# Kernel tuning notes

Measured on AMD Instinct MI355X. Metric: run time of the kernel, lower is better.

## Reference

```python
import jax, jax.numpy as jnp
import numpy as np

K = 40          # neighbors, from __init__ default
EPS_BN = 1e-5   # BatchNorm eps; eval mode with running_mean=0, running_var=1


def knn_idx(x, k):
    # x: (B, C, N) -> indices (B, N, k) of k nearest neighbors (incl. self)
    xx = jnp.sum(x * x, axis=1)                      # (B, N)
    inner = jnp.einsum('bcn,bcm->bnm', x, x)         # (B, N, N)
    neg_dist = 2.0 * inner - xx[:, :, None] - xx[:, None, :]
    return jax.lax.top_k(neg_dist, k)[1]


def get_graph_feature(x, k):
    # DGCNN dynamic graph feature: (B, C, N) -> (B, 2C, N, k)
    idx = knn_idx(x, k)                              # (B, N, k) int
    xt = jnp.transpose(x, (0, 2, 1))                 # (B, N, C)
    nbr = jax.vmap(lambda f, i: f[i])(xt, idx)       # (B, N, k, C)
    ctr = xt[:, :, None, :]
    feat = jnp.concatenate([nbr - ctr, jnp.broadcast_to(ctr, nbr.shape)], axis=-1)
    return jnp.transpose(feat, (0, 3, 1, 2))         # (B, 2C, N, k)


def bn_affine(x, g, b, ch_axis=1):
    # eval-mode BatchNorm with running_mean=0, running_var=1
    shape = [1] * x.ndim
    shape[ch_axis] = -1
    scale = (g / jnp.sqrt(1.0 + EPS_BN)).reshape(shape)
    return x * scale + b.reshape(shape)


def conv_bn_lrelu2d(x, w, g, b):
    # 1x1 Conv2d (no bias) + BN2d + LeakyReLU(0.2); x: (B, Cin, N, k)
    y = jnp.einsum('oi,bink->bonk', w, x)
    return jax.nn.leaky_relu(bn_affine(y, g, b, 1), 0.2)


def sa_layer(x, qk, vw, vb, tw, tb, g, b):
    # PCT-style offset self-attention; q and k share weights. x: (B, C, N)
    xq = jnp.einsum('oc,bcn->bno', qk, x)            # (B, N, C/4)
    xk = jnp.einsum('oc,bcn->bon', qk, x)            # (B, C/4, N)
    xv = jnp.einsum('oc,bcn->bon', vw, x) + vb[None, :, None]
    energy = jnp.einsum('bno,bom->bnm', xq, xk)      # (B, N, N)
    attn = jax.nn.softmax(energy, axis=-1)
    attn = attn / (1e-9 + jnp.sum(attn, axis=1, keepdims=True))
    xr = jnp.einsum('bcn,bnm->bcm', xv, attn)        # (B, C, N)
    d = x - xr
    dr = jnp.einsum('oc,bcn->bon', tw, d) + tb[None, :, None]
    return x + jax.nn.relu(bn_affine(dr, g, b, 1))


def setup_inputs() -> dict:
    key = jax.random.key(0)
    ks = jax.random.split(key, 16)
    s = 0.05
    d = {
        'x': jax.random.normal(ks[0], (8, 2048, 3), jnp.float32),
        'w1': jax.random.normal(ks[1], (64, 6), jnp.float32) * s,
        'g1': jnp.ones((64,), jnp.float32), 'b1': jnp.zeros((64,), jnp.float32),
        'w2': jax.random.normal(ks[2], (64, 64), jnp.float32) * s,
        'g2': jnp.ones((64,), jnp.float32), 'b2': jnp.zeros((64,), jnp.float32),
        'w3': jax.random.normal(ks[3], (64, 128), jnp.float32) * s,
        'g3': jnp.ones((64,), jnp.float32), 'b3': jnp.zeros((64,), jnp.float32),
        'w4': jax.random.normal(ks[4], (64, 64), jnp.float32) * s,
        'g4': jnp.ones((64,), jnp.float32), 'b4': jnp.zeros((64,), jnp.float32),
        'w5': jax.random.normal(ks[5], (64, 128), jnp.float32) * s,
        'g5': jnp.ones((64,), jnp.float32), 'b5': jnp.zeros((64,), jnp.float32),
        'sa_qk': jax.random.normal(ks[6], (4, 32, 128), jnp.float32) * s,
        'sa_v': jax.random.normal(ks[7], (4, 128, 128), jnp.float32) * s,
        'sa_vb': jnp.zeros((4, 128), jnp.float32),
        'sa_t': jax.random.normal(ks[8], (4, 128, 128), jnp.float32) * s,
        'sa_tb': jnp.zeros((4, 128), jnp.float32),
        'sa_g': jnp.ones((4, 128), jnp.float32),
        'sa_b': jnp.zeros((4, 128), jnp.float32),
        'fuse_w': jax.random.normal(ks[9], (256, 512), jnp.float32) * s,
        'fuse_g': jnp.ones((256,), jnp.float32),
        'fuse_b': jnp.zeros((256,), jnp.float32),
    }
    return d


def reference(x, w1, g1, b1, w2, g2, b2, w3, g3, b3, w4, g4, b4, w5, g5, b5,
              sa_qk, sa_v, sa_vb, sa_t, sa_tb, sa_g, sa_b,
              fuse_w, fuse_g, fuse_b):
    xc = jnp.transpose(x, (0, 2, 1))                 # (B, 3, N)
    f = get_graph_feature(xc, K)                     # (B, 6, N, k)
    f = conv_bn_lrelu2d(f, w1, g1, b1)
    f = conv_bn_lrelu2d(f, w2, g2, b2)
    x1 = jnp.max(f, axis=-1)                         # (B, 64, N)
    f = get_graph_feature(x1, K)                     # (B, 128, N, k)
    f = conv_bn_lrelu2d(f, w3, g3, b3)
    f = conv_bn_lrelu2d(f, w4, g4, b4)
    x2 = jnp.max(f, axis=-1)                         # (B, 64, N)
    h = jnp.concatenate([x1, x2], axis=1)            # (B, 128, N)
    outs = []
    for i in range(4):
        h = sa_layer(h, sa_qk[i], sa_v[i], sa_vb[i], sa_t[i], sa_tb[i], sa_g[i], sa_b[i])
        outs.append(h)
    cat = jnp.concatenate(outs, axis=1)              # (B, 512, N)
    y = jnp.einsum('oi,bin->bon', fuse_w, cat)       # (B, 256, N)
    return jax.nn.leaky_relu(bn_affine(y, fuse_g, fuse_b, 1), 0.2)
```

## Files before the change

kernel.cpp:

```cpp
#include <hip/hip_runtime.h>

#define Bb 8
#define Nn 2048
#define Kk 40
#define HS (128*Nn)

__device__ __forceinline__ unsigned f2o(float f){
  unsigned u = __float_as_uint(f);
  return (u & 0x80000000u) ? ~u : (u | 0x80000000u);
}

__device__ __forceinline__ void wave_top40(float* d, int lane, int* op){
  float gv[4]; int gs[4];
  #pragma unroll
  for (int g=0; g<4; ++g){
    float bv = d[g*8]; int bs = g*8;
    #pragma unroll
    for (int j=1;j<8;++j){
      float v = d[g*8+j];
      if (v > bv){ bv = v; bs = g*8+j; }
    }
    gv[g]=bv; gs[g]=bs;
  }
  for (int t=0; t<Kk; ++t){
    float bv = gv[0]; int bs = gs[0];
    if (gv[1] > bv){ bv=gv[1]; bs=gs[1]; }
    if (gv[2] > bv){ bv=gv[2]; bs=gs[2]; }
    if (gv[3] > bv){ bv=gv[3]; bs=gs[3]; }
    int bm = bs*64 + lane;
    unsigned long long key = ((unsigned long long)f2o(bv) << 32) | (unsigned)(~bm);
    #pragma unroll
    for (int s=32;s>0;s>>=1){
      unsigned long long o = __shfl_xor(key, s, 64);
      if (o > key) key = o;
    }
    int wm = (int)(~(unsigned)key);
    if (lane == 0) op[t] = wm;
    bool mine = ((wm & 63) == lane);
    int wsl = wm >> 6;
    if (mine){
      int G = wsl >> 3;
      #pragma unroll
      for (int g=0; g<4; ++g){
        if (g == G){
          float nv = -__builtin_inff(); int ns = g*8;
          #pragma unroll
          for (int j=0;j<8;++j){
            float v = d[g*8+j];
            if (g*8+j == wsl) v = -__builtin_inff();
            d[g*8+j] = v;
            if (v > nv){ nv=v; ns=g*8+j; }
          }
          gv[g]=nv; gs[g]=ns;
        }
      }
    }
  }
}

__device__ __forceinline__ void wave_top40_g(float* d, int lane, int* op){
  float gv[4]; int gs[4];
  #pragma unroll
  for (int g=0; g<4; ++g){
    float bv = d[g*8]; int bs = g*8;
    #pragma unroll
    for (int j=1;j<8;++j){
      float v = d[g*8+j];
      if (v > bv){ bv = v; bs = g*8+j; }
    }
    gv[g]=bv; gs[g]=bs;
  }
  for (int t=0; t<Kk; ++t){
    float bv = gv[0]; int bs = gs[0];
    if (gv[1] > bv){ bv=gv[1]; bs=gs[1]; }
    if (gv[2] > bv){ bv=gv[2]; bs=gs[2]; }
    if (gv[3] > bv){ bv=gv[3]; bs=gs[3]; }
    int bm = ((bs>>2)<<8) + lane*4 + (bs&3);
    unsigned long long key = ((unsigned long long)f2o(bv) << 32) | (unsigned)(~bm);
    #pragma unroll
    for (int s=32;s>0;s>>=1){
      unsigned long long o = __shfl_xor(key, s, 64);
      if (o > key) key = o;
    }
    int wm = (int)(~(unsigned)key);
    if (lane == 0) op[t] = wm;
    bool mine = (((wm>>2) & 63) == lane);
    int wsl = ((wm>>8)<<2) | (wm & 3);
    if (mine){
      int G = wsl >> 3;
      #pragma unroll
      for (int g=0; g<4; ++g){
        if (g == G){
          float nv = -__builtin_inff(); int ns = g*8;
          #pragma unroll
          for (int j=0;j<8;++j){
            float v = d[g*8+j];
            if (g*8+j == wsl) v = -__builtin_inff();
            d[g*8+j] = v;
            if (v > nv){ nv=v; ns=g*8+j; }
          }
          gv[g]=nv; gs[g]=ns;
        }
      }
    }
  }
}

__global__ __launch_bounds__(256) void k_xx1(const float* __restrict__ x, float* __restrict__ XX){
  int e = blockIdx.x*256 + threadIdx.x;
  if (e >= Bb*Nn) return;
  float p0 = x[e*3+0], p1 = x[e*3+1], p2 = x[e*3+2];
  XX[e] = __fadd_rn(__fadd_rn(__fmul_rn(p0,p0), __fmul_rn(p1,p1)), __fmul_rn(p2,p2));
}

__global__ __launch_bounds__(256) void k_prep_wt(const float* __restrict__ w1, const float* __restrict__ w2,
                                                 const float* __restrict__ w3, const float* __restrict__ w4,
                                                 const float* __restrict__ fw,
                                                 float* __restrict__ W1T, float* __restrict__ W2T,
                                                 float* __restrict__ W3T, float* __restrict__ W4T,
                                                 float* __restrict__ FWT){
  int e = blockIdx.x*256 + threadIdx.x;
  if (e < 384)   { int i=e/64,  c=e%64;  W1T[e] = w1[c*6+i];    return; } e -= 384;
  if (e < 4096)  { int i=e/64,  c=e%64;  W2T[e] = w2[c*64+i];   return; } e -= 4096;
  if (e < 8192)  { int i=e/64,  c=e%64;  W3T[e] = w3[c*128+i];  return; } e -= 8192;
  if (e < 4096)  { int i=e/64,  c=e%64;  W4T[e] = w4[c*64+i];   return; } e -= 4096;
  if (e < 131072){ int i=e/256, o=e%256; FWT[e] = fw[o*512+i];  return; }
}

__global__ __launch_bounds__(256) void k_knn1(const float* __restrict__ P, const float* __restrict__ XX,
                                              int* __restrict__ IDX){
  int blk = blockIdx.x;
  int b = blk >> 9;
  int w = threadIdx.x >> 6, lane = threadIdx.x & 63;
  int n = (blk & 511)*4 + w;
  const float* Pb = P + b*Nn*3;
  const float* xb = XX + b*Nn;
  __shared__ float Pl[Nn*3];
  __shared__ float Xl[Nn];
  for (int e = threadIdx.x; e < Nn*3; e += 256) Pl[e] = Pb[e];
  for (int e = threadIdx.x; e < Nn; e += 256) Xl[e] = xb[e];
  __syncthreads();
  float c0 = Pl[n*3+0], c1 = Pl[n*3+1], c2 = Pl[n*3+2];
  float xn = Xl[n];
  float d[32];
  #pragma unroll
  for (int j=0;j<32;++j){
    int m = j*64 + lane;
    float a0 = Pl[m*3+0], a1 = Pl[m*3+1], a2 = Pl[m*3+2];
    float in_ = __fadd_rn(__fadd_rn(__fmul_rn(c0,a0), __fmul_rn(c1,a1)), __fmul_rn(c2,a2));
    d[j] = __fsub_rn(__fsub_rn(__fmul_rn(2.0f,in_), xn), Xl[m]);
  }
  wave_top40(d, lane, IDX + (b*Nn+n)*Kk);
}

__global__ __launch_bounds__(64) void k_ec1(const float* __restrict__ P, const int* __restrict__ IDX,
                                            const float* __restrict__ W1T, const float* __restrict__ W2T,
                                            const float* __restrict__ g1, const float* __restrict__ b1,
                                            const float* __restrict__ g2, const float* __restrict__ b2,
                                            float* __restrict__ X1T){
  int e = blockIdx.x;
  int b = e >> 11;
  int lane = threadIdx.x;
  __shared__ float dC[Kk*4];
  __shared__ __align__(16) float y1L[64*44];
  float c0 = P[e*3+0], c1 = P[e*3+1], c2 = P[e*3+2];
  if (lane < Kk) {
    int idx = IDX[e*Kk + lane] & (Nn-1);
    const float* pn = P + (b*Nn + idx)*3;
    dC[lane*4+0] = __fsub_rn(pn[0], c0);
    dC[lane*4+1] = __fsub_rn(pn[1], c1);
    dC[lane*4+2] = __fsub_rn(pn[2], c2);
  }
  __syncthreads();
  float w10 = W1T[0*64+lane], w11 = W1T[1*64+lane], w12 = W1T[2*64+lane];
  float w13 = W1T[3*64+lane], w14 = W1T[4*64+lane], w15 = W1T[5*64+lane];
  float p3 = __fmul_rn(w13,c0), p4 = __fmul_rn(w14,c1), p5 = __fmul_rn(w15,c2);
  float s1 = __fdiv_rn(g1[lane], __fsqrt_rn(1.0f + 1e-5f));
  float o1 = b1[lane];
  for (int k=0;k<Kk;++k){
    float t = __fmul_rn(w10, dC[k*4+0]);
    t = __fadd_rn(t, __fmul_rn(w11, dC[k*4+1]));
    t = __fadd_rn(t, __fmul_rn(w12, dC[k*4+2]));
    t = __fadd_rn(t, p3); t = __fadd_rn(t, p4); t = __fadd_rn(t, p5);
    float y = __fadd_rn(__fmul_rn(t, s1), o1);
    y = (y >= 0.0f) ? y : __fmul_rn(0.2f, y);
    y1L[lane*44+k] = y;
  }
  __syncthreads();
  float4 q[10];
  #pragma unroll
  for (int k4=0;k4<10;++k4) q[k4] = make_float4(0.f,0.f,0.f,0.f);
  for (int i=0;i<64;++i){
    float w = W2T[i*64+lane];
    const float4* yp = (const float4*)&y1L[i*44];
    #pragma unroll
    for (int k4=0;k4<10;++k4){
      float4 yv = yp[k4];
      q[k4].x = __fadd_rn(q[k4].x, __fmul_rn(w, yv.x));
      q[k4].y = __fadd_rn(q[k4].y, __fmul_rn(w, yv.y));
      q[k4].z = __fadd_rn(q[k4].z, __fmul_rn(w, yv.z));
      q[k4].w = __fadd_rn(q[k4].w, __fmul_rn(w, yv.w));
    }
  }
  float s2 = __fdiv_rn(g2[lane], __fsqrt_rn(1.0f + 1e-5f));
  float o2 = b2[lane];
  float mx = -__builtin_inff();
  #pragma unroll
  for (int k4=0;k4<10;++k4){
    float vs[4] = {q[k4].x, q[k4].y, q[k4].z, q[k4].w};
    #pragma unroll
    for (int j=0;j<4;++j){
      float y = __fadd_rn(__fmul_rn(vs[j], s2), o2);
      y = (y >= 0.0f) ? y : __fmul_rn(0.2f, y);
      mx = fmaxf(mx, y);
    }
  }
  X1T[e*64 + lane] = mx;
}

__global__ __launch_bounds__(256) void k_xx2(const float* __restrict__ X1T, float* __restrict__ XX2){
  int e = blockIdx.x*256 + threadIdx.x;
  const float* r = X1T + e*64;
  float a = 0.f;
  for (int c=0;c<64;++c) a = __fadd_rn(a, __fmul_rn(r[c], r[c]));
  XX2[e] = a;
}

__global__ __launch_bounds__(256) void k_knn2(const float* __restrict__ X1C, const float* __restrict__ XX2,
                                              int* __restrict__ IDX){
  int blk = blockIdx.x;
  int b = blk >> 8;
  int n0 = (blk & 255) << 3;
  int w = threadIdx.x >> 6, lane = threadIdx.x & 63;
  __shared__ float qL[8*64];
  for (int e=threadIdx.x; e<512; e+=256){
    int q = e >> 6, c = e & 63;
    qL[e] = X1C[b*HS + c*Nn + n0 + q];
  }
  __syncthreads();
  float4 a0[8], a1[8];
  #pragma unroll
  for (int j=0;j<8;++j){
    a0[j] = make_float4(0.f,0.f,0.f,0.f);
    a1[j] = make_float4(0.f,0.f,0.f,0.f);
  }
  for (int c=0;c<64;++c){
    const float4* row = (const float4*)(X1C + b*HS + c*Nn);
    float q0 = qL[(w*2+0)*64 + c];
    float q1 = qL[(w*2+1)*64 + c];
    #pragma unroll
    for (int j=0;j<8;++j){
      float4 v = row[j*64 + lane];
      a0[j].x = __fadd_rn(a0[j].x, __fmul_rn(q0, v.x));
      a0[j].y = __fadd_rn(a0[j].y, __fmul_rn(q0, v.y));
      a0[j].z = __fadd_rn(a0[j].z, __fmul_rn(q0, v.z));
      a0[j].w = __fadd_rn(a0[j].w, __fmul_rn(q0, v.w));
      a1[j].x = __fadd_rn(a1[j].x, __fmul_rn(q1, v.x));
      a1[j].y = __fadd_rn(a1[j].y, __fmul_rn(q1, v.y));
      a1[j].z = __fadd_rn(a1[j].z, __fmul_rn(q1, v.z));
      a1[j].w = __fadd_rn(a1[j].w, __fmul_rn(q1, v.w));
    }
  }
  const float* xb = XX2 + b*Nn;
  const float4* xb4 = (const float4*)xb;
  {
    int n = n0 + w*2 + 0;
    float xn = xb[n];
    float d[32];
    #pragma unroll
    for (int j=0;j<8;++j){
      float4 xm = xb4[j*64 + lane];
      d[j*4+0] = __fsub_rn(__fsub_rn(__fmul_rn(2.0f, a0[j].x), xn), xm.x);
      d[j*4+1] = __fsub_rn(__fsub_rn(__fmul_rn(2.0f, a0[j].y), xn), xm.y);
      d[j*4+2] = __fsub_rn(__fsub_rn(__fmul_rn(2.0f, a0[j].z), xn), xm.z);
      d[j*4+3] = __fsub_rn(__fsub_rn(__fmul_rn(2.0f, a0[j].w), xn), xm.w);
    }
    wave_top40_g(d, lane, IDX + (b*Nn + n)*Kk);
  }
  {
    int n = n0 + w*2 + 1;
    float xn = xb[n];
    float d[32];
    #pragma unroll
    for (int j=0;j<8;++j){
      float4 xm = xb4[j*64 + lane];
      d[j*4+0] = __fsub_rn(__fsub_rn(__fmul_rn(2.0f, a1[j].x), xn), xm.x);
      d[j*4+1] = __fsub_rn(__fsub_rn(__fmul_rn(2.0f, a1[j].y), xn), xm.y);
      d[j*4+2] = __fsub_rn(__fsub_rn(__fmul_rn(2.0f, a1[j].z), xn), xm.z);
      d[j*4+3] = __fsub_rn(__fsub_rn(__fmul_rn(2.0f, a1[j].w), xn), xm.w);
    }
    wave_top40_g(d, lane, IDX + (b*Nn + n)*Kk);
  }
}

__global__ __launch_bounds__(64) void k_ec2(const float* __restrict__ X1T, const int* __restrict__ IDX,
                                            const float* __restrict__ W3T, const float* __restrict__ W4T,
                                            const float* __restrict__ g3, const float* __restrict__ b3,
                                            const float* __restrict__ g4, const float* __restrict__ b4,
                                            float* __restrict__ X2T){
  int e = blockIdx.x; int b = e >> 11; int lane = threadIdx.x;
  __shared__ __align__(16) float dL[64*44];
  __shared__ float ctrL[64];
  float ctr = X1T[e*64 + lane];
  ctrL[lane] = ctr;
  __syncthreads();
  for (int k=0;k<Kk;++k){
    int idx = IDX[e*Kk + k] & (Nn-1);
    dL[lane*44 + k] = X1T[(b*Nn+idx)*64 + lane] - ctr;
  }
  __syncthreads();
  float base = 0.f;
  for (int i=0;i<64;++i) base = fmaf(W3T[(64+i)*64 + lane], ctrL[i], base);
  float4 q[10];
  #pragma unroll
  for (int k4=0;k4<10;++k4) q[k4] = make_float4(base,base,base,base);
  for (int i=0;i<64;++i){
    float w = W3T[i*64 + lane];
    const float4* dp = (const float4*)&dL[i*44];
    #pragma unroll
    for (int k4=0;k4<10;++k4){
      float4 d = dp[k4];
      q[k4].x = fmaf(w, d.x, q[k4].x);
      q[k4].y = fmaf(w, d.y, q[k4].y);
      q[k4].z = fmaf(w, d.z, q[k4].z);
      q[k4].w = fmaf(w, d.w, q[k4].w);
    }
  }
  float s3 = g3[lane] / sqrtf(1.0f+1e-5f);
  float o3 = b3[lane];
  __syncthreads();
  #pragma unroll
  for (int k4=0;k4<10;++k4){
    float4 y;
    y.x = q[k4].x*s3 + o3; y.x = (y.x>=0.f)?y.x:0.2f*y.x;
    y.y = q[k4].y*s3 + o3; y.y = (y.y>=0.f)?y.y:0.2f*y.y;
    y.z = q[k4].z*s3 + o3; y.z = (y.z>=0.f)?y.z:0.2f*y.z;
    y.w = q[k4].w*s3 + o3; y.w = (y.w>=0.f)?y.w:0.2f*y.w;
    *(float4*)&dL[lane*44 + k4*4] = y;
  }
  __syncthreads();
  float4 p[10];
  #pragma unroll
  for (int k4=0;k4<10;++k4) p[k4] = make_float4(0.f,0.f,0.f,0.f);
  for (int i=0;i<64;++i){
    float w = W4T[i*64 + lane];
    const float4* yp = (const float4*)&dL[i*44];
    #pragma unroll
    for (int k4=0;k4<10;++k4){
      float4 yv = yp[k4];
      p[k4].x = fmaf(w, yv.x, p[k4].x);
      p[k4].y = fmaf(w, yv.y, p[k4].y);
      p[k4].z = fmaf(w, yv.z, p[k4].z);
      p[k4].w = fmaf(w, yv.w, p[k4].w);
    }
  }
  float s4 = g4[lane] / sqrtf(1.0f+1e-5f);
  float o4 = b4[lane];
  float mx = -__builtin_inff();
  #pragma unroll
  for (int k4=0;k4<10;++k4){
    float vs[4] = {p[k4].x, p[k4].y, p[k4].z, p[k4].w};
    #pragma unroll
    for (int j=0;j<4;++j){
      float y = vs[j]*s4 + o4;
      y = (y>=0.f)?y:0.2f*y;
      mx = fmaxf(mx, y);
    }
  }
  X2T[e*64 + lane] = mx;
}

__global__ __launch_bounds__(256) void k_tr(const float* __restrict__ src, float* __restrict__ dst){
  int b = blockIdx.x >> 5; int n0 = (blockIdx.x & 31) << 6;
  __shared__ float t[64*65];
  for (int e=threadIdx.x; e<4096; e+=256){
    int r = e >> 6, c = e & 63;
    t[r*65+c] = src[(b*Nn + n0 + r)*64 + c];
  }
  __syncthreads();
  for (int e=threadIdx.x; e<4096; e+=256){
    int c = e >> 6, r = e & 63;
    dst[b*HS + c*Nn + n0 + r] = t[r*65+c];
  }
}

__global__ __launch_bounds__(256) void k_sa_a(const float* __restrict__ IN,
                                              const float* __restrict__ QKw, const float* __restrict__ Vw,
                                              const float* __restrict__ Vb,
                                              float* __restrict__ QX, float* __restrict__ XV){
  int blk = blockIdx.x;
  int part = blk & 1; int nt = (blk >> 1) & 31; int b = blk >> 6;
  int n0 = nt << 6;
  int w = threadIdx.x >> 6, lane = threadIdx.x & 63;
  __shared__ __align__(16) float xl[128*64];
  for (int e=threadIdx.x; e<2048; e+=256){
    int c = e >> 4, j4 = (e & 15) << 2;
    *(float4*)&xl[(c<<6) + j4] = *(const float4*)&IN[b*HS + c*Nn + n0 + j4];
  }
  __syncthreads();
  for (int i=0;i<20;++i){
    int r = part*80 + w*20 + i;
    const float4* wp4;
    if (r < 32) wp4 = (const float4*)(QKw + r*128);
    else        wp4 = (const float4*)(Vw + (r-32)*128);
    float a = 0.f;
    #pragma unroll
    for (int c4=0;c4<32;++c4){
      float4 wv = wp4[c4];
      a = fmaf(wv.x, xl[(c4*4+0)*64 + lane], a);
      a = fmaf(wv.y, xl[(c4*4+1)*64 + lane], a);
      a = fmaf(wv.z, xl[(c4*4+2)*64 + lane], a);
      a = fmaf(wv.w, xl[(c4*4+3)*64 + lane], a);
    }
    if (r < 32) QX[(b*32+r)*Nn + n0 + lane] = a;
    else { int o = r-32; XV[(b*128+o)*Nn + n0 + lane] = a + Vb[o]; }
  }
}

__global__ __launch_bounds__(256) void k_sa_b(const float* __restrict__ QX,
                                              float* __restrict__ RMP, float* __restrict__ RSP){
  int blk = blockIdx.x;
  int b = blk >> 6, sub = blk & 63;
  int ncn = sub >> 3, mcn = sub & 7;
  int n = ncn*256 + threadIdx.x;
  float q[32];
  #pragma unroll
  for (int o=0;o<32;++o) q[o] = QX[(b*32+o)*Nn + n];
  __shared__ __align__(16) float qt[32*128];
  float mr = -__builtin_inff(), lr = 0.f;
  int m0 = mcn*256;
  for (int t=0;t<2;++t){
    for (int e=threadIdx.x; e<1024; e+=256){
      int o = e >> 5, mm4 = (e & 31) << 2;
      *(float4*)&qt[(o<<7) + mm4] = *(const float4*)&QX[(b*32+o)*Nn + m0 + t*128 + mm4];
    }
    __syncthreads();
    for (int mm=0;mm<128;mm+=4){
      float e0=0.f, e1=0.f, e2=0.f, e3=0.f;
      #pragma unroll
      for (int o=0;o<32;++o){
        float qo=q[o];
        float4 qv = *(const float4*)&qt[o*128+mm];
        e0 = fmaf(qo, qv.x, e0);
        e1 = fmaf(qo, qv.y, e1);
        e2 = fmaf(qo, qv.z, e2);
        e3 = fmaf(qo, qv.w, e3);
      }
      if (e0 > mr){ lr = lr*expf(mr-e0) + 1.f; mr = e0; } else lr += expf(e0-mr);
      if (e1 > mr){ lr = lr*expf(mr-e1) + 1.f; mr = e1; } else lr += expf(e1-mr);
      if (e2 > mr){ lr = lr*expf(mr-e2) + 1.f; mr = e2; } else lr += expf(e2-mr);
      if (e3 > mr){ lr = lr*expf(mr-e3) + 1.f; mr = e3; } else lr += expf(e3-mr);
    }
    __syncthreads();
  }
  RMP[(b*Nn+n)*8 + mcn] = mr;
  RSP[(b*Nn+n)*8 + mcn] = lr;
}

__global__ __launch_bounds__(256) void k_sa_b2(const float* __restrict__ RMP, const float* __restrict__ RSP,
                                               float* __restrict__ RMX, float* __restrict__ RSM){
  int e = blockIdx.x*256 + threadIdx.x;
  float M = -__builtin_inff();
  #pragma unroll
  for (int i=0;i<8;++i) M = fmaxf(M, RMP[e*8+i]);
  float l = 0.f;
  #pragma unroll
  for (int i=0;i<8;++i) l += RSP[e*8+i]*expf(RMP[e*8+i]-M);
  RMX[e] = M; RSM[e] = l;
}

#define SM_QM 0
#define SM_QN 1024
#define SM_XV 2048
#define SM_SL 6272
#define SM_MX 7296
#define SM_RL 7328

__global__ __launch_bounds__(256) void k_sa_cm(const float* __restrict__ QX, const float* __restrict__ XV,
                                               const float* __restrict__ RMAX, const float* __restrict__ RSUM,
                                               float* __restrict__ PP, float* __restrict__ CSP){
  int blk = blockIdx.x;
  int part = blk & 1, mt = (blk >> 1) & 63, b = blk >> 7;
  int m0 = mt << 5;
  int tid = threadIdx.x;
  int nnp = tid >> 4, mmp = tid & 15;
  int tc = tid >> 3, tm8 = tid & 7;
  __shared__ __align__(16) float sm[7360];
  {
    int o = tid >> 3, mm4 = (tid & 7) << 2;
    *(float4*)&sm[SM_QM + (o<<5) + mm4] = *(const float4*)&QX[(b*32+o)*Nn + m0 + mm4];
  }
  float acc[4][4];
  #pragma unroll
  for (int ci=0;ci<4;++ci){
    #pragma unroll
    for (int mi=0;mi<4;++mi) acc[ci][mi] = 0.f;
  }
  float csr = 0.f;
  int it0 = part*32;
  for (int it=it0; it<it0+32; ++it){
    int nb = it*32;
    __syncthreads();
    {
      int o = tid >> 3, nn4 = (tid & 7) << 2;
      *(float4*)&sm[SM_QN + (o<<5) + nn4] = *(const float4*)&QX[(b*32+o)*Nn + nb + nn4];
    }
    for (int e=tid; e<1024; e+=256){
      int c = e >> 3, nn4 = (e & 7) << 2;
      float4 v = *(const float4*)&XV[(b*128+c)*Nn + nb + nn4];
      sm[SM_XV + (nn4+0)*132 + c] = v.x;
      sm[SM_XV + (nn4+1)*132 + c] = v.y;
      sm[SM_XV + (nn4+2)*132 + c] = v.z;
      sm[SM_XV + (nn4+3)*132 + c] = v.w;
    }
    if (tid < 32){ sm[SM_MX+tid] = RMAX[b*Nn + nb + tid]; sm[SM_RL+tid] = 1.0f / RSUM[b*Nn + nb + tid]; }
    __syncthreads();
    float e00=0.f, e01=0.f, e10=0.f, e11=0.f;
    #pragma unroll
    for (int o=0;o<32;++o){
      float2 qn = *(const float2*)&sm[SM_QN + o*32 + nnp*2];
      float2 qm = *(const float2*)&sm[SM_QM + o*32 + mmp*2];
      e00 = fmaf(qn.x, qm.x, e00);
      e01 = fmaf(qn.x, qm.y, e01);
      e10 = fmaf(qn.y, qm.x, e10);
      e11 = fmaf(qn.y, qm.y, e11);
    }
    float mx0 = sm[SM_MX + nnp*2],   rl0 = sm[SM_RL + nnp*2];
    float mx1 = sm[SM_MX + nnp*2+1], rl1 = sm[SM_RL + nnp*2+1];
    float2 s0; s0.x = expf(e00-mx0)*rl0; s0.y = expf(e01-mx0)*rl0;
    float2 s1; s1.x = expf(e10-mx1)*rl1; s1.y = expf(e11-mx1)*rl1;
    *(float2*)&sm[SM_SL + (nnp*2  )*32 + mmp*2] = s0;
    *(float2*)&sm[SM_SL + (nnp*2+1)*32 + mmp*2] = s1;
    __syncthreads();
    if (tid < 32){
      #pragma unroll
      for (int nn=0;nn<32;++nn) csr += sm[SM_SL + nn*32 + tid];
    }
    #pragma unroll 8
    for (int nn=0;nn<32;++nn){
      float4 xv4 = *(const float4*)&sm[SM_XV + nn*132 + tc*4];
      float4 s4  = *(const float4*)&sm[SM_SL + nn*32  + tm8*4];
      acc[0][0] = fmaf(xv4.x, s4.x, acc[0][0]);
      acc[0][1] = fmaf(xv4.x, s4.y, acc[0][1]);
      acc[0][2] = fmaf(xv4.x, s4.z, acc[0][2]);
      acc[0][3] = fmaf(xv4.x, s4.w, acc[0][3]);
      acc[1][0] = fmaf(xv4.y, s4.x, acc[1][0]);
      acc[1][1] = fmaf(xv4.y, s4.y, acc[1][1]);
      acc[1][2] = fmaf(xv4.y, s4.z, acc[1][2]);
      acc[1][3] = fmaf(xv4.y, s4.w, acc[1][3]);
      acc[2][0] = fmaf(xv4.z, s4.x, acc[2][0]);
      acc[2][1] = fmaf(xv4.z, s4.y, acc[2][1]);
      acc[2][2] = fmaf(xv4.z, s4.z, acc[2][2]);
      acc[2][3] = fmaf(xv4.z, s4.w, acc[2][3]);
      acc[3][0] = fmaf(xv4.w, s4.x, acc[3][0]);
      acc[3][1] = fmaf(xv4.w, s4.y, acc[3][1]);
      acc[3][2] = fmaf(xv4.w, s4.z, acc[3][2]);
      acc[3][3] = fmaf(xv4.w, s4.w, acc[3][3]);
    }
  }
  int slot = (b*64 + mt)*2 + part;
  #pragma unroll
  for (int ci=0;ci<4;++ci){
    int c = tc*4 + ci;
    *(float4*)&PP[slot*4096 + c*32 + tm8*4] =
      make_float4(acc[ci][0], acc[ci][1], acc[ci][2], acc[ci][3]);
  }
  if (tid < 32) CSP[slot*32 + tid] = csr;
}

__global__ __launch_bounds__(256) void k_sa_cc(const float* IN,
                                               const float* __restrict__ PP, const float* __restrict__ CSP,
                                               const float* __restrict__ Tw, const float* __restrict__ Tb,
                                               const float* __restrict__ Gs, const float* __restrict__ Bs,
                                               float* OUT){
  int blk = blockIdx.x;
  int mt = blk & 63, b = blk >> 6;
  int m0 = mt << 5;
  int tid = threadIdx.x;
  int tc = tid >> 3, tm8 = tid & 7;
  __shared__ __align__(16) float sm[4128];
  int s0 = (b*64 + mt)*2, s1 = s0 + 1;
  if (tid < 32) sm[4096 + tid] = CSP[s0*32 + tid] + CSP[s1*32 + tid];
  __syncthreads();
  #pragma unroll
  for (int ci=0;ci<4;++ci){
    int c = tc*4 + ci;
    float4 p0 = *(const float4*)&PP[s0*4096 + c*32 + tm8*4];
    float4 p1 = *(const float4*)&PP[s1*4096 + c*32 + tm8*4];
    float4 inv = *(const float4*)&IN[b*HS + c*Nn + m0 + tm8*4];
    float am[4] = {p0.x+p1.x, p0.y+p1.y, p0.z+p1.z, p0.w+p1.w};
    float ivs[4] = {inv.x, inv.y, inv.z, inv.w};
    #pragma unroll
    for (int mi=0;mi<4;++mi){
      int ml = tm8*4 + mi;
      float cs = sm[4096 + ml];
      float xr = am[mi] / (1e-9f + cs);
      sm[c*32 + ml] = ivs[mi] - xr;
    }
  }
  __syncthreads();
  int hw = tid >> 5, m = tid & 31;
  float sroot = sqrtf(1.0f + 1e-5f);
  for (int oo=0; oo<16; ++oo){
    int o = oo*8 + hw;
    const float4* twp = (const float4*)(Tw + o*128);
    float a = 0.f;
    #pragma unroll
    for (int c4=0;c4<32;++c4){
      float4 wv = twp[c4];
      a = fmaf(wv.x, sm[(c4*4+0)*32 + m], a);
      a = fmaf(wv.y, sm[(c4*4+1)*32 + m], a);
      a = fmaf(wv.z, sm[(c4*4+2)*32 + m], a);
      a = fmaf(wv.w, sm[(c4*4+3)*32 + m], a);
    }
    a += Tb[o];
    float y = a * (Gs[o] / sroot) + Bs[o];
    y = fmaxf(y, 0.f);
    OUT[b*HS + o*Nn + m0 + m] = IN[b*HS + o*Nn + m0 + m] + y;
  }
}

__global__ __launch_bounds__(256) void k_fuse_part(const float* __restrict__ Hc, const float* __restrict__ FWT,
                                                   float* __restrict__ ACC, int l, int init, int fin,
                                                   const float* __restrict__ FGF, const float* __restrict__ FBF){
  int blk = blockIdx.x;
  int hf = blk & 1; int nt = (blk >> 1) & 31; int b = blk >> 6;
  int n0 = nt << 6;
  int w = threadIdx.x >> 6, lane = threadIdx.x & 63;
  __shared__ __align__(16) float xt[128*64];
  for (int e=threadIdx.x; e<2048; e+=256){
    int c = e >> 4, j4 = (e & 15) << 2;
    *(float4*)&xt[(c<<6) + j4] = *(const float4*)&Hc[(b*128 + c)*Nn + n0 + j4];
  }
  __syncthreads();
  float4 a[8];
  #pragma unroll
  for (int j=0;j<8;++j) a[j] = make_float4(0.f,0.f,0.f,0.f);
  int ob = hf*128 + w*32;
  for (int c=0;c<128;++c){
    float xv = xt[c*64 + lane];
    const float4* wr = (const float4*)(FWT + (l*128+c)*256 + ob);
    #pragma unroll
    for (int j4=0;j4<8;++j4){
      float4 wv = wr[j4];
      a[j4].x = fmaf(wv.x, xv, a[j4].x);
      a[j4].y = fmaf(wv.y, xv, a[j4].y);
      a[j4].z = fmaf(wv.z, xv, a[j4].z);
      a[j4].w = fmaf(wv.w, xv, a[j4].w);
    }
  }
  float sroot = sqrtf(1.0f + 1e-5f);
  #pragma unroll
  for (int j4=0;j4<8;++j4){
    float vs[4] = {a[j4].x, a[j4].y, a[j4].z, a[j4].w};
    #pragma unroll
    for (int qq=0;qq<4;++qq){
      int o = ob + j4*4 + qq;
      int idx = (b*256 + o)*Nn + n0 + lane;
      float v = init ? vs[qq] : (ACC[idx] + vs[qq]);
      if (fin){
        float y = v * (FGF[o] / sroot) + FBF[o];
        y = (y >= 0.f) ? y : 0.2f*y;
        ACC[idx] = y;
      } else {
        ACC[idx] = v;
      }
    }
  }
}

extern "C" void kernel_launch(void* const* d_in, const int* in_sizes, int n_in,
                              void* d_out, int out_size, void* d_ws, size_t ws_size,
                              hipStream_t stream) {
  const float* X   = (const float*)d_in[0];
  const float* w1  = (const float*)d_in[1];
  const float* g1  = (const float*)d_in[2];
  const float* b1  = (const float*)d_in[3];
  const float* w2  = (const float*)d_in[4];
  const float* g2  = (const float*)d_in[5];
  const float* b2_ = (const float*)d_in[6];
  const float* w3  = (const float*)d_in[7];
  const float* g3  = (const float*)d_in[8];
  const float* b3  = (const float*)d_in[9];
  const float* w4  = (const float*)d_in[10];
  const float* g4  = (const float*)d_in[11];
  const float* b4  = (const float*)d_in[12];
  const float* qk  = (const float*)d_in[16];
  const float* sv  = (const float*)d_in[17];
  const float* svb = (const float*)d_in[18];
  const float* st  = (const float*)d_in[19];
  const float* stb = (const float*)d_in[20];
  const float* sg  = (const float*)d_in[21];
  const float* sb  = (const float*)d_in[22];
  const float* fw  = (const float*)d_in[23];
  const float* fg  = (const float*)d_in[24];
  const float* fb  = (const float*)d_in[25];

  float* ws = (float*)d_ws;
  float* H    = ws + 0;
  float* QXb  = ws + 2097152;
  float* XVb  = ws + 2621440;
  float* RMP  = ws + 4718592;
  float* RSP  = ws + 4849664;
  float* RMX  = ws + 4980736;
  float* RSM  = ws + 4997120;
  float* XX   = ws + 2146304;
  int*   IDX  = (int*)(ws + 2162688);
  float* X1T  = ws + 2818048;
  float* X2T  = ws + 3866624;
  float* C0   = ws + 5013504;
  float* W1T = C0 + 0;
  float* W2T = C0 + 384;
  float* W3T = C0 + 4480;
  float* W4T = C0 + 12672;
  float* FWT = C0 + 16768;
  float* PP  = ws + 5161344;
  float* CSP = ws + 9355648;
  float* ACC = (float*)d_out;

  k_xx1<<<64,256,0,stream>>>(X, XX);
  k_prep_wt<<<578,256,0,stream>>>(w1,w2,w3,w4,fw, W1T,W2T,W3T,W4T,FWT);
  k_knn1<<<4096,256,0,stream>>>(X, XX, IDX);
  k_ec1<<<16384,64,0,stream>>>(X, IDX, W1T, W2T, g1,b1,g2,b2_, X1T);
  k_xx2<<<64,256,0,stream>>>(X1T, XX);
  k_tr<<<256,256,0,stream>>>(X1T, H);
  k_knn2<<<2048,256,0,stream>>>(H, XX, IDX);
  k_ec2<<<16384,64,0,stream>>>(X1T, IDX, W3T, W4T, g3,b3,g4,b4, X2T);
  k_tr<<<256,256,0,stream>>>(X2T, H + 64*Nn);

  for (int l=0;l<4;++l){
    k_sa_a<<<512,256,0,stream>>>(H, qk + l*4096, sv + l*16384, svb + l*128, QXb, XVb);
    k_sa_b<<<512,256,0,stream>>>(QXb, RMP, RSP);
    k_sa_b2<<<64,256,0,stream>>>(RMP, RSP, RMX, RSM);
    k_sa_cm<<<1024,256,0,stream>>>(QXb, XVb, RMX, RSM, PP, CSP);
    k_sa_cc<<<512,256,0,stream>>>(H, PP, CSP,
                                  st + l*16384, stb + l*128, sg + l*128, sb + l*128, H);
    k_fuse_part<<<512,256,0,stream>>>(H, FWT, ACC, l, (l==0)?1:0, (l==3)?1:0, fg, fb);
  }
}
```

Baseline: 2.461 ms.

## Interleave two top-k selections and register-prefetch attention tiles

The kNN kernel now runs the two rows' top-40 selections interleaved in one routine, so the shuffle reductions of two independent chains overlap and hide latency. The attention kernel prefetches the next tile's Q, V and row-stat values into registers during the current tile's compute, then stores them to shared memory at the next iteration. Both changes raise register pressure, which may reduce occupancy.

Result: no change. 2.429 ms (-1.3%).

```diff
diff --git a/kernel.cpp b/kernel.cpp
--- a/kernel.cpp
+++ b/kernel.cpp
@@ -58,48 +58,85 @@
   }
 }
 
-__device__ __forceinline__ void wave_top40_g(float* d, int lane, int* op){
-  float gv[4]; int gs[4];
+__device__ __forceinline__ void wave_top40_g2(float* d0, float* d1, int lane,
+                                              int* op0, int* op1){
+  float gv0[4], gv1[4]; int gs0[4], gs1[4];
   #pragma unroll
   for (int g=0; g<4; ++g){
-    float bv = d[g*8]; int bs = g*8;
+    float bv0 = d0[g*8]; int bs0 = g*8;
+    float bv1 = d1[g*8]; int bs1 = g*8;
     #pragma unroll
     for (int j=1;j<8;++j){
-      float v = d[g*8+j];
-      if (v > bv){ bv = v; bs = g*8+j; }
-    }
-    gv[g]=bv; gs[g]=bs;
+      float v0 = d0[g*8+j];
+      if (v0 > bv0){ bv0 = v0; bs0 = g*8+j; }
+      float v1 = d1[g*8+j];
+      if (v1 > bv1){ bv1 = v1; bs1 = g*8+j; }
+    }
+    gv0[g]=bv0; gs0[g]=bs0;
+    gv1[g]=bv1; gs1[g]=bs1;
   }
   for (int t=0; t<Kk; ++t){
-    float bv = gv[0]; int bs = gs[0];
-    if (gv[1] > bv){ bv=gv[1]; bs=gs[1]; }
-    if (gv[2] > bv){ bv=gv[2]; bs=gs[2]; }
-    if (gv[3] > bv){ bv=gv[3]; bs=gs[3]; }
-    int bm = ((bs>>2)<<8) + lane*4 + (bs&3);
-    unsigned long long key = ((unsigned long long)f2o(bv) << 32) | (unsigned)(~bm);
+    float bv0 = gv0[0]; int bs0 = gs0[0];
+    if (gv0[1] > bv0){ bv0=gv0[1]; bs0=gs0[1]; }
+    if (gv0[2] > bv0){ bv0=gv0[2]; bs0=gs0[2]; }
+    if (gv0[3] > bv0){ bv0=gv0[3]; bs0=gs0[3]; }
+    float bv1 = gv1[0]; int bs1 = gs1[0];
+    if (gv1[1] > bv1){ bv1=gv1[1]; bs1=gs1[1]; }
+    if (gv1[2] > bv1){ bv1=gv1[2]; bs1=gs1[2]; }
+    if (gv1[3] > bv1){ bv1=gv1[3]; bs1=gs1[3]; }
+    int bm0 = ((bs0>>2)<<8) + lane*4 + (bs0&3);
+    int bm1 = ((bs1>>2)<<8) + lane*4 + (bs1&3);
+    unsigned long long key0 = ((unsigned long long)f2o(bv0) << 32) | (unsigned)(~bm0);
+    unsigned long long key1 = ((unsigned long long)f2o(bv1) << 32) | (unsigned)(~bm1);
     #pragma unroll
     for (int s=32;s>0;s>>=1){
-      unsigned long long o = __shfl_xor(key, s, 64);
-      if (o > key) key = o;
-    }
-    int wm = (int)(~(unsigned)key);
-    if (lane == 0) op[t] = wm;
-    bool mine = (((wm>>2) & 63) == lane);
-    int wsl = ((wm>>8)<<2) | (wm & 3);
-    if (mine){
-      int G = wsl >> 3;
-      #pragma unroll
-      for (int g=0; g<4; ++g){
-        if (g == G){
-          float nv = -__builtin_inff(); int ns = g*8;
-          #pragma unroll
-          for (int j=0;j<8;++j){
-            float v = d[g*8+j];
-            if (g*8+j == wsl) v = -__builtin_inff();
-            d[g*8+j] = v;
-            if (v > nv){ nv=v; ns=g*8+j; }
+      unsigned long long o0 = __shfl_xor(key0, s, 64);
+      unsigned long long o1 = __shfl_xor(key1, s, 64);
+      if (o0 > key0) key0 = o0;
+      if (o1 > key1) key1 = o1;
+    }
+    int wm0 = (int)(~(unsigned)key0);
+    int wm1 = (int)(~(unsigned)key1);
+    if (lane == 0){ op0[t] = wm0; op1[t] = wm1; }
+    {
+      bool mine = (((wm0>>2) & 63) == lane);
+      int wsl = ((wm0>>8)<<2) | (wm0 & 3);
+      if (mine){
+        int G = wsl >> 3;
+        #pragma unroll
+        for (int g=0; g<4; ++g){
+          if (g == G){
+            float nv = -__builtin_inff(); int ns = g*8;
+            #pragma unroll
+            for (int j=0;j<8;++j){
+              float v = d0[g*8+j];
+              if (g*8+j == wsl) v = -__builtin_inff();
+              d0[g*8+j] = v;
+              if (v > nv){ nv=v; ns=g*8+j; }
+            }
+            gv0[g]=nv; gs0[g]=ns;
           }
-          gv[g]=nv; gs[g]=ns;
+        }
+      }
+    }
+    {
+      bool mine = (((wm1>>2) & 63) == lane);
+      int wsl = ((wm1>>8)<<2) | (wm1 & 3);
+      if (mine){
+        int G = wsl >> 3;
+        #pragma unroll
+        for (int g=0; g<4; ++g){
+          if (g == G){
+            float nv = -__builtin_inff(); int ns = g*8;
+            #pragma unroll
+            for (int j=0;j<8;++j){
+              float v = d1[g*8+j];
+              if (g*8+j == wsl) v = -__builtin_inff();
+              d1[g*8+j] = v;
+              if (v > nv){ nv=v; ns=g*8+j; }
+            }
+            gv1[g]=nv; gs1[g]=ns;
+          }
         }
       }
     }
@@ -263,34 +300,24 @@
   }
   const float* xb = XX2 + b*Nn;
   const float4* xb4 = (const float4*)xb;
-  {
-    int n = n0 + w*2 + 0;
-    float xn = xb[n];
-    float d[32];
-    #pragma unroll
-    for (int j=0;j<8;++j){
-      float4 xm = xb4[j*64 + lane];
-      d[j*4+0] = __fsub_rn(__fsub_rn(__fmul_rn(2.0f, a0[j].x), xn), xm.x);
-      d[j*4+1] = __fsub_rn(__fsub_rn(__fmul_rn(2.0f, a0[j].y), xn), xm.y);
-      d[j*4+2] = __fsub_rn(__fsub_rn(__fmul_rn(2.0f, a0[j].z), xn), xm.z);
-      d[j*4+3] = __fsub_rn(__fsub_rn(__fmul_rn(2.0f, a0[j].w), xn), xm.w);
-    }
-    wave_top40_g(d, lane, IDX + (b*Nn + n)*Kk);
-  }
-  {
-    int n = n0 + w*2 + 1;
-    float xn = xb[n];
-    float d[32];
-    #pragma unroll
-    for (int j=0;j<8;++j){
-      float4 xm = xb4[j*64 + lane];
-      d[j*4+0] = __fsub_rn(__fsub_rn(__fmul_rn(2.0f, a1[j].x), xn), xm.x);
-      d[j*4+1] = __fsub_rn(__fsub_rn(__fmul_rn(2.0f, a1[j].y), xn), xm.y);
-      d[j*4+2] = __fsub_rn(__fsub_rn(__fmul_rn(2.0f, a1[j].z), xn), xm.z);
-      d[j*4+3] = __fsub_rn(__fsub_rn(__fmul_rn(2.0f, a1[j].w), xn), xm.w);
-    }
-    wave_top40_g(d, lane, IDX + (b*Nn + n)*Kk);
-  }
+  int na = n0 + w*2 + 0;
+  int nb = n0 + w*2 + 1;
+  float xna = xb[na];
+  float xnb = xb[nb];
+  float d0[32], d1[32];
+  #pragma unroll
+  for (int j=0;j<8;++j){
+    float4 xm = xb4[j*64 + lane];
+    d0[j*4+0] = __fsub_rn(__fsub_rn(__fmul_rn(2.0f, a0[j].x), xna), xm.x);
+    d0[j*4+1] = __fsub_rn(__fsub_rn(__fmul_rn(2.0f, a0[j].y), xna), xm.y);
+    d0[j*4+2] = __fsub_rn(__fsub_rn(__fmul_rn(2.0f, a0[j].z), xna), xm.z);
+    d0[j*4+3] = __fsub_rn(__fsub_rn(__fmul_rn(2.0f, a0[j].w), xna), xm.w);
+    d1[j*4+0] = __fsub_rn(__fsub_rn(__fmul_rn(2.0f, a1[j].x), xnb), xm.x);
+    d1[j*4+1] = __fsub_rn(__fsub_rn(__fmul_rn(2.0f, a1[j].y), xnb), xm.y);
+    d1[j*4+2] = __fsub_rn(__fsub_rn(__fmul_rn(2.0f, a1[j].z), xnb), xm.z);
+    d1[j*4+3] = __fsub_rn(__fsub_rn(__fmul_rn(2.0f, a1[j].w), xnb), xm.w);
+  }
+  wave_top40_g2(d0, d1, lane, IDX + (b*Nn + na)*Kk, IDX + (b*Nn + nb)*Kk);
 }
 
 __global__ __launch_bounds__(64) void k_ec2(const float* __restrict__ X1T, const int* __restrict__ IDX,
@@ -498,22 +525,34 @@
   }
   float csr = 0.f;
   int it0 = part*32;
+  int o_q = tid >> 3, nn4_q = (tid & 7) << 2;
+  float4 rQN;
+  float4 rXV[4];
+  float rMX = 0.f, rRS = 0.f;
+  {
+    int nb = it0*32;
+    rQN = *(const float4*)&QX[(b*32+o_q)*Nn + nb + nn4_q];
+    #pragma unroll
+    for (int u=0;u<4;++u){
+      int e = tid + u*256;
+      int c = e >> 3, nn4 = (e & 7) << 2;
+      rXV[u] = *(const float4*)&XV[(b*128+c)*Nn + nb + nn4];
+    }
+    if (tid < 32){ rMX = RMAX[b*Nn + nb + tid]; rRS = RSUM[b*Nn + nb + tid]; }
+  }
   for (int it=it0; it<it0+32; ++it){
-    int nb = it*32;
     __syncthreads();
-    {
-      int o = tid >> 3, nn4 = (tid & 7) << 2;
-      *(float4*)&sm[SM_QN + (o<<5) + nn4] = *(const float4*)&QX[(b*32+o)*Nn + nb + nn4];
-    }
-    for (int e=tid; e<1024; e+=256){
+    *(float4*)&sm[SM_QN + (o_q<<5) + nn4_q] = rQN;
+    #pragma unroll
+    for (int u=0;u<4;++u){
+      int e = tid + u*256;
       int c = e >> 3, nn4 = (e & 7) << 2;
-      float4 v = *(const float4*)&XV[(b*128+c)*Nn + nb + nn4];
-      sm[SM_XV + (nn4+0)*132 + c] = v.x;
-      sm[SM_XV + (nn4+1)*132 + c] = v.y;
-      sm[SM_XV + (nn4+2)*132 + c] = v.z;
-      sm[SM_XV + (nn4+3)*132 + c] = v.w;
-    }
-    if (tid < 32){ sm[SM_MX+tid] = RMAX[b*Nn + nb + tid]; sm[SM_RL+tid] = 1.0f / RSUM[b*Nn + nb + tid]; }
+      sm[SM_XV + (nn4+0)*132 + c] = rXV[u].x;
+      sm[SM_XV + (nn4+1)*132 + c] = rXV[u].y;
+      sm[SM_XV + (nn4+2)*132 + c] = rXV[u].z;
+      sm[SM_XV + (nn4+3)*132 + c] = rXV[u].w;
+    }
+    if (tid < 32){ sm[SM_MX+tid] = rMX; sm[SM_RL+tid] = 1.0f / rRS; }
     __syncthreads();
     float e00=0.f, e01=0.f, e10=0.f, e11=0.f;
     #pragma unroll
@@ -531,6 +570,17 @@
     float2 s1; s1.x = expf(e10-mx1)*rl1; s1.y = expf(e11-mx1)*rl1;
     *(float2*)&sm[SM_SL + (nnp*2  )*32 + mmp*2] = s0;
     *(float2*)&sm[SM_SL + (nnp*2+1)*32 + mmp*2] = s1;
+    if (it+1 < it0+32){
+      int nb2 = (it+1)*32;
+      rQN = *(const float4*)&QX[(b*32+o_q)*Nn + nb2 + nn4_q];
+      #pragma unroll
+      for (int u=0;u<4;++u){
+        int e = tid + u*256;
+        int c = e >> 3, nn4 = (e & 7) << 2;
+        rXV[u] = *(const float4*)&XV[(b*128+c)*Nn + nb2 + nn4];
+      }
+      if (tid < 32){ rMX = RMAX[b*Nn + nb2 + tid]; rRS = RSUM[b*Nn + nb2 + tid]; }
+    }
     __syncthreads();
     if (tid < 32){
       #pragma unroll
```
